# Kernel tuning notes

Hardware: AMD Instinct MI355X
Metric: run time of the kernel (lower is better)

The kernel has to match this reference:

```python
import jax, jax.numpy as jnp
import numpy as np

HIDDEN = 1024
NUM_HEADS = 16
HEAD_SIZE = HIDDEN // NUM_HEADS


def setup_inputs() -> dict:
    key = jax.random.key(0)
    ks = jax.random.split(key, 5)
    B, S = 2, 2048
    x = jax.random.normal(ks[0], (B, S, HIDDEN), dtype=jnp.float32)
    # nn.Linear(hidden, 3*hidden): weight stored (in, out) for x @ W
    scale_qkv = 1.0 / np.sqrt(HIDDEN)
    w_qkv = jax.random.uniform(ks[1], (HIDDEN, 3 * HIDDEN), minval=-scale_qkv, maxval=scale_qkv, dtype=jnp.float32)
    b_qkv = jax.random.uniform(ks[2], (3 * HIDDEN,), minval=-scale_qkv, maxval=scale_qkv, dtype=jnp.float32)
    w_o = jax.random.uniform(ks[3], (HIDDEN, HIDDEN), minval=-scale_qkv, maxval=scale_qkv, dtype=jnp.float32)
    b_o = jax.random.uniform(ks[4], (HIDDEN,), minval=-scale_qkv, maxval=scale_qkv, dtype=jnp.float32)
    return {"x": x, "w_qkv": w_qkv, "b_qkv": b_qkv, "w_o": w_o, "b_o": b_o}


def reference(x, w_qkv, b_qkv, w_o, b_o):
    B, S, H = x.shape
    qkv = x @ w_qkv + b_qkv  # (B, S, 3H)
    q, k, v = jnp.split(qkv, 3, axis=-1)
    # (B, S, H) -> (B, nheads, S, head_size)
    def heads(t):
        return t.reshape(B, S, NUM_HEADS, HEAD_SIZE).transpose(0, 2, 1, 3)
    q, k, v = heads(q), heads(k), heads(v)
    scores = jnp.einsum('bhqd,bhkd->bhqk', q, k) / np.sqrt(HEAD_SIZE).astype(np.float32)
    causal = jnp.tril(jnp.ones((S, S), dtype=bool))  # k <= q
    scores = jnp.where(causal, scores, -jnp.inf)
    probs = jax.nn.softmax(scores, axis=-1)
    out = jnp.einsum('bhqk,bhkd->bqhd', probs, v).reshape(B, S, H)
    return out @ w_o + b_o
```

## Files before the change

kernel.cpp:

```cpp
#include <hip/hip_runtime.h>
#include <stdint.h>


typedef __bf16 bf16;
typedef __attribute__((ext_vector_type(8))) __bf16 bf16x8;
typedef __attribute__((ext_vector_type(4))) __bf16 bf16x4;
typedef __attribute__((ext_vector_type(4))) float floatx4;
typedef __attribute__((ext_vector_type(16))) float floatx16;
typedef __attribute__((ext_vector_type(4))) unsigned int uint4v;
typedef __attribute__((ext_vector_type(2))) unsigned int uint2v;

#define SCL 0.18033688011112042f

__device__ __forceinline__ floatx4 mfma_bf16(bf16x8 a, bf16x8 b, floatx4 c) {
  return __builtin_amdgcn_mfma_f32_16x16x32_bf16(a, b, c, 0, 0, 0);
}

__device__ __forceinline__ floatx16 mfma32(bf16x8 a, bf16x8 b, floatx16 c) {
  return __builtin_amdgcn_mfma_f32_32x32x16_bf16(a, b, c, 0, 0, 0);
}

__device__ __forceinline__ void cp_g2l_16(const bf16* g, bf16* l) {
  __builtin_amdgcn_global_load_lds(
      (const __attribute__((address_space(1))) void*)g,
      (__attribute__((address_space(3))) void*)l, 16, 0, 0);
}

__device__ __forceinline__ floatx16 zero16() {
  floatx16 z;
#pragma unroll
  for (int i = 0; i < 16; ++i) z[i] = 0.f;
  return z;
}

__device__ __forceinline__ uint32_t pack2(float lo, float hi2) {
  union { bf16 h[2]; uint32_t u; } x;
  x.h[0] = (bf16)lo; x.h[1] = (bf16)hi2;
  return x.u;
}

__device__ __forceinline__ uint2v permswap(uint32_t a, uint32_t b) {
  return __builtin_amdgcn_permlane32_swap(a, b, false, false);
}

__device__ __forceinline__ bf16x8 mk_pf(uint32_t w0, uint32_t w1, uint32_t w2,
                                        uint32_t w3) {
  union { uint4v u; bf16x8 v; } c;
  c.u = (uint4v){w0, w1, w2, w3};
  return c.v;
}

__global__ __launch_bounds__(256) void prep_kernel(
    const float* __restrict__ x, bf16* __restrict__ xb,
    const float* __restrict__ w_qkv, bf16* __restrict__ wqkvt,
    const float* __restrict__ w_o, bf16* __restrict__ wot) {
  const int b = blockIdx.x;
  const int tid = threadIdx.x;
  if (b < 4096) {
    const int i = (b * 256 + tid) * 4;
    floatx4 v = *(const floatx4*)(x + i);
    bf16x4 o;
    o[0] = (bf16)v[0]; o[1] = (bf16)v[1]; o[2] = (bf16)v[2]; o[3] = (bf16)v[3];
    *(bf16x4*)(xb + i) = o;
    return;
  }
  __shared__ float tile[32][33];
  const float* W; bf16* Wt; int K, N, n0, k0;
  if (b < 7168) {
    const int bb = b - 4096;
    W = w_qkv; Wt = wqkvt; K = 1024; N = 3072;
    n0 = (bb % 96) * 32; k0 = (bb / 96) * 32;
  } else {
    const int bb = b - 7168;
    W = w_o; Wt = wot; K = 1024; N = 1024;
    n0 = (bb & 31) * 32; k0 = (bb >> 5) * 32;
  }
  const int tx = tid & 31, ty = tid >> 5;
  for (int i = 0; i < 4; ++i)
    tile[ty + 8 * i][tx] = W[(size_t)(k0 + ty + 8 * i) * N + n0 + tx];
  __syncthreads();
  for (int i = 0; i < 4; ++i)
    Wt[(size_t)(n0 + ty + 8 * i) * K + k0 + tx] = (bf16)tile[tx][ty + 8 * i];
}

template <int MODE, int MI>
__global__ __launch_bounds__(256, 3) void gemm_bt_kernel(
    const bf16* __restrict__ A, const bf16* __restrict__ Bt,
    const float* __restrict__ bias, float* __restrict__ outF,
    bf16* __restrict__ qb, bf16* __restrict__ kb, bf16* __restrict__ vtb,
    int N, int K) {
  constexpr int BM = MI * 32;
  __shared__ bf16 As[BM * 32];
  __shared__ bf16 Bs[128 * 32];
  const int tid = threadIdx.x;
  const int w = tid >> 6, lane = tid & 63;
  const int l16 = lane & 15, quad = lane >> 4;
  const int m0 = blockIdx.y * BM, n0 = blockIdx.x * 128;
  const int wm = (w & 1) * (BM / 2), wn = (w >> 1) * 64;

  const int r4 = lane >> 2, c4 = lane & 3;
  const int jj = (c4 - r4 - (r4 >> 2)) & 3;
  const int arow = w * (BM / 4) + r4;
  const bf16* Ag = A + (size_t)(m0 + arow) * K + jj * 8;
  bf16* Al = As + arow * 32 + c4 * 8;
  const int brow = w * 32 + r4;
  const bf16* Bg = Bt + (size_t)(n0 + brow) * K + jj * 8;
  bf16* Bl = Bs + brow * 32 + c4 * 8;

  floatx4 acc[MI][4];
#pragma unroll
  for (int i = 0; i < MI; ++i)
#pragma unroll
    for (int j = 0; j < 4; ++j) acc[i][j] = (floatx4){0.f, 0.f, 0.f, 0.f};

  for (int k0 = 0; k0 < K; k0 += 32) {
    __syncthreads();
    cp_g2l_16(Ag + k0, Al);
    if (MI == 4) cp_g2l_16(Ag + (size_t)16 * K + k0, Al + 16 * 32);
    cp_g2l_16(Bg + k0, Bl);
    cp_g2l_16(Bg + (size_t)16 * K + k0, Bl + 16 * 32);
    __syncthreads();
    bf16x8 af[MI], bfr[4];
#pragma unroll
    for (int i = 0; i < MI; ++i) {
      const int R = wm + i * 16 + l16;
      af[i] = *(const bf16x8*)(&As[R * 32 + ((quad + R + (R >> 2)) & 3) * 8]);
    }
#pragma unroll
    for (int j = 0; j < 4; ++j) {
      const int Rb = wn + j * 16 + l16;
      bfr[j] = *(const bf16x8*)(&Bs[Rb * 32 + ((quad + Rb + (Rb >> 2)) & 3) * 8]);
    }
#pragma unroll
    for (int i = 0; i < MI; ++i)
#pragma unroll
      for (int j = 0; j < 4; ++j)
        acc[i][j] = mfma_bf16(af[i], bfr[j], acc[i][j]);
  }

#pragma unroll
  for (int i = 0; i < MI; ++i)
#pragma unroll
    for (int j = 0; j < 4; ++j) {
      const int nn = n0 + wn + j * 16 + l16;
      const float bv = bias[nn];
      const int mbase = m0 + wm + i * 16 + quad * 4;
      if (MODE == 1) {
#pragma unroll
        for (int r = 0; r < 4; ++r)
          outF[(size_t)(mbase + r) * N + nn] = acc[i][j][r] + bv;
      } else {
        const int which = nn >> 10;
        const int rem = nn & 1023;
        const int h = rem >> 6, d = rem & 63;
        const int b = mbase >> 11, s = mbase & 2047;
        const size_t bh = (size_t)(b * 16 + h);
        if (which == 2) {
          bf16x4 pk;
#pragma unroll
          for (int r = 0; r < 4; ++r) pk[r] = (bf16)(acc[i][j][r] + bv);
          *(bf16x4*)(vtb + (bh * 64 + d) * 2048 + s) = pk;
        } else if (which == 0) {
#pragma unroll
          for (int r = 0; r < 4; ++r)
            qb[(bh * 2048 + s + r) * 64 + d] = (bf16)((acc[i][j][r] + bv) * SCL);
        } else {
#pragma unroll
          for (int r = 0; r < 4; ++r)
            kb[(bh * 2048 + s + r) * 64 + d] = (bf16)(acc[i][j][r] + bv);
        }
      }
    }
}

__global__ __launch_bounds__(256, 4) void attn_kernel(
    const bf16* __restrict__ Qb, const bf16* __restrict__ Kb,
    const bf16* __restrict__ Vtb, bf16* __restrict__ attnb) {
  __shared__ bf16 Ks[3][4096];
  __shared__ bf16 Vs[2][4096];
  const int bid = blockIdx.x;
  const int c = bid & 255, qq = bid >> 8;
  const int bh = c & 31;
  const int kk = c >> 5;
  const int g = (qq == 0) ? kk : (qq == 1) ? 31 - kk
              : (qq == 2) ? 8 + kk : 23 - kk;
  const int tid = threadIdx.x;
  const int w = tid >> 6, lane = tid & 63;
  const int l31 = lane & 31, hi = lane >> 5;
  const int strip = w >> 1, ms = w & 1;
  const int q0s = g * 64 + strip * 32;
  const int b = bh >> 4, h = bh & 15;
  const int nt = g + 1;

  const bf16* Qh = Qb + (size_t)bh * 2048 * 64;
  const bf16* Kh = Kb + (size_t)bh * 2048 * 64;
  const bf16* Vh = Vtb + (size_t)bh * 64 * 2048;

  const int c0 = tid, c1 = tid + 256;
  const int kof0 = (c0 >> 3) * 64 + ((((c0 & 7) - (c0 >> 3)) & 7) * 8);
  const int kof1 = (c1 >> 3) * 64 + ((((c1 & 7) - (c1 >> 3)) & 7) * 8);
  const int vof0 = (c0 >> 3) * 2048 + ((((c0 & 7) - (c0 >> 3)) & 7) * 8);
  const int vof1 = (c1 >> 3) * 2048 + ((((c1 & 7) - (c1 >> 3)) & 7) * 8);

  bf16x8 qf[4];
  {
    const bf16* Qr = Qh + (size_t)(q0s + l31) * 64 + hi * 8;
#pragma unroll
    for (int kd = 0; kd < 4; ++kd) qf[kd] = *(const bf16x8*)(Qr + kd * 16);
  }
  bf16x8 ones;
#pragma unroll
  for (int j = 0; j < 8; ++j) ones[j] = (bf16)1.0f;

  floatx16 O0 = zero16(), O1 = zero16(), Ol = zero16();

  {
    const int k1 = (1 < nt) ? 1 : 0;
    cp_g2l_16(Kh + kof0, &Ks[0][c0 * 8]);
    cp_g2l_16(Kh + kof1, &Ks[0][c1 * 8]);
    cp_g2l_16(Kh + (size_t)k1 * 4096 + kof0, &Ks[1][c0 * 8]);
    cp_g2l_16(Kh + (size_t)k1 * 4096 + kof1, &Ks[1][c1 * 8]);
    cp_g2l_16(Vh + vof0, &Vs[0][c0 * 8]);
    cp_g2l_16(Vh + vof1, &Vs[0][c1 * 8]);
    asm volatile("s_waitcnt vmcnt(4)" ::: "memory");
    __builtin_amdgcn_sched_barrier(0);
  }

  int kr = 0;
  for (int t = 0; t < nt; ++t) {
    __builtin_amdgcn_s_barrier();
    __builtin_amdgcn_sched_barrier(0);

    {
      const int tk = (t + 2 < nt) ? t + 2 : 0;
      const int tv = (t + 1 < nt) ? t + 1 : 0;
      const int kst = (kr >= 1) ? kr - 1 : 2;
      cp_g2l_16(Kh + (size_t)tk * 4096 + kof0, &Ks[kst][c0 * 8]);
      cp_g2l_16(Kh + (size_t)tk * 4096 + kof1, &Ks[kst][c1 * 8]);
      cp_g2l_16(Vh + (size_t)tv * 64 + vof0, &Vs[(t + 1) & 1][c0 * 8]);
      cp_g2l_16(Vh + (size_t)tv * 64 + vof1, &Vs[(t + 1) & 1][c1 * 8]);
    }

    const bool diag = (t == g);
    if (!(diag && strip == 0 && ms == 1)) {
      const bf16* KsC = &Ks[kr][0];

      floatx16 sf = zero16();
      const int row = ms * 32 + l31;
      __builtin_amdgcn_s_setprio(1);
#pragma unroll
      for (int kd = 0; kd < 4; ++kd) {
        bf16x8 kf = *(const bf16x8*)(
            &KsC[row * 64 + (((kd * 2 + hi) + row) & 7) * 8]);
        sf = mfma32(kf, qf[kd], sf);
      }
      __builtin_amdgcn_s_setprio(0);

      float e[16];
#pragma unroll
      for (int r = 0; r < 16; ++r) {
        float s = sf[r];
        if (diag) {
          const int kc = t * 64 + ms * 32 + (r & 3) + 8 * (r >> 2) + 4 * hi;
          s = (kc <= q0s + l31) ? s : -1e30f;
        }
        e[r] = __builtin_amdgcn_exp2f(s);
      }

      uint32_t W[8];
#pragma unroll
      for (int i = 0; i < 8; ++i) W[i] = pack2(e[2 * i], e[2 * i + 1]);
      uint2v s0 = permswap(W[0], W[2]);
      uint2v s1 = permswap(W[1], W[3]);
      bf16x8 pa = mk_pf(s0.x, s1.x, s0.y, s1.y);
      uint2v s2 = permswap(W[4], W[6]);
      uint2v s3 = permswap(W[5], W[7]);
      bf16x8 pb = mk_pf(s2.x, s3.x, s2.y, s3.y);

      asm volatile("s_waitcnt vmcnt(4)" ::: "memory");
      __builtin_amdgcn_sched_barrier(0);

      const bf16* VsC = &Vs[t & 1][0];
      const int ksA = ms * 2, ksB = ms * 2 + 1;
      const int r0 = l31, r1 = 32 + l31;
      bf16x8 va0 = *(const bf16x8*)(&VsC[r0 * 64 + (((ksA * 2 + hi) + r0) & 7) * 8]);
      bf16x8 va1 = *(const bf16x8*)(&VsC[r1 * 64 + (((ksA * 2 + hi) + r1) & 7) * 8]);
      bf16x8 vb0 = *(const bf16x8*)(&VsC[r0 * 64 + (((ksB * 2 + hi) + r0) & 7) * 8]);
      bf16x8 vb1 = *(const bf16x8*)(&VsC[r1 * 64 + (((ksB * 2 + hi) + r1) & 7) * 8]);

      __builtin_amdgcn_s_setprio(1);
      O0 = mfma32(pa, va0, O0);
      O1 = mfma32(pa, va1, O1);
      Ol = mfma32(pa, ones, Ol);
      O0 = mfma32(pb, vb0, O0);
      O1 = mfma32(pb, vb1, O1);
      Ol = mfma32(pb, ones, Ol);
      __builtin_amdgcn_s_setprio(0);
    }
    kr = (kr == 2) ? 0 : kr + 1;
  }

  __syncthreads();
  float* fO = (float*)(&Ks[0][0]);
  float* fL = (float*)(&Vs[0][0]);
  if (ms == 1) {
#pragma unroll
    for (int r = 0; r < 16; ++r) {
      const int ql = (r & 3) + 8 * (r >> 2) + 4 * hi;
      fO[strip * 2048 + ql * 64 + l31] = O0[r];
      fO[strip * 2048 + ql * 64 + 32 + l31] = O1[r];
      if (l31 == 0) fL[strip * 32 + ql] = Ol[r];
    }
  }
  __syncthreads();
  if (ms == 0) {
#pragma unroll
    for (int r = 0; r < 16; ++r) {
      const int ql = (r & 3) + 8 * (r >> 2) + 4 * hi;
      const float o0 = O0[r] + fO[strip * 2048 + ql * 64 + l31];
      const float o1 = O1[r] + fO[strip * 2048 + ql * 64 + 32 + l31];
      const float inv = 1.f / (Ol[r] + fL[strip * 32 + ql]);
      bf16* dst = attnb + ((size_t)(b * 2048 + q0s + ql)) * 1024 + h * 64;
      dst[l31] = (bf16)(o0 * inv);
      dst[32 + l31] = (bf16)(o1 * inv);
    }
  }
}

extern "C" void kernel_launch(void* const* d_in, const int* in_sizes, int n_in,
                              void* d_out, int out_size, void* d_ws, size_t ws_size,
                              hipStream_t stream) {
  const float* x     = (const float*)d_in[0];
  const float* w_qkv = (const float*)d_in[1];
  const float* b_qkv = (const float*)d_in[2];
  const float* w_o   = (const float*)d_in[3];
  const float* b_o   = (const float*)d_in[4];
  float* out = (float*)d_out;

  char* ws = (char*)d_ws;
  bf16* xb    = (bf16*)ws; ws += (size_t)4096 * 1024 * 2;
  bf16* wqkvt = (bf16*)ws; ws += (size_t)3072 * 1024 * 2;
  bf16* wot   = (bf16*)ws; ws += (size_t)1024 * 1024 * 2;
  bf16* qb    = (bf16*)ws; ws += (size_t)32 * 2048 * 64 * 2;
  bf16* kb    = (bf16*)ws; ws += (size_t)32 * 2048 * 64 * 2;
  bf16* vtb   = (bf16*)ws; ws += (size_t)32 * 2048 * 64 * 2;
  bf16* attnb = (bf16*)ws; ws += (size_t)4096 * 1024 * 2;

  prep_kernel<<<8192, 256, 0, stream>>>(x, xb, w_qkv, wqkvt, w_o, wot);
  gemm_bt_kernel<0, 4><<<dim3(24, 32), 256, 0, stream>>>(
      xb, wqkvt, b_qkv, nullptr, qb, kb, vtb, 3072, 1024);
  attn_kernel<<<1024, 256, 0, stream>>>(qb, kb, vtb, attnb);
  gemm_bt_kernel<1, 2><<<dim3(8, 64), 256, 0, stream>>>(
      attnb, wot, b_o, out, nullptr, nullptr, nullptr, 1024, 1024);
}
```

Measured before the change: 171.2 us.

## Software-pipeline PV MFMAs by one tile to overlap with QK and exp

The P·V MFMAs for tile t-1 are deferred into iteration t, so they sit between the QK^T MFMAs and the exp/pack work of tile t, with a drain after the loop. The V fragments for the previous tile are read from LDS right after the barrier. The goal is to hide the exp/pack latency and LDS read latency behind independent matrix work instead of serialising QK, softmax and PV within each iteration. In exchange, P must stay live across iterations, which costs registers. V is read from the buffer that the next prefetch overwrites in the same iteration, and only the barrier before those reads orders them against other waves' async loads, so there is a possible LDS read/write race.

```diff
diff --git a/kernel.cpp b/kernel.cpp
--- a/kernel.cpp
+++ b/kernel.cpp
@@ -226,9 +226,23 @@
     __builtin_amdgcn_sched_barrier(0);
   }
 
+  const int ksA = ms * 2, ksB = ms * 2 + 1;
+  const int r0v = l31, r1v = 32 + l31;
+  bf16x8 paS, pbS;
+  int havePrev = 0;
   int kr = 0;
   for (int t = 0; t < nt; ++t) {
     __builtin_amdgcn_s_barrier();
+    __builtin_amdgcn_sched_barrier(0);
+
+    bf16x8 va0, va1, vb0, vb1;
+    if (havePrev) {
+      const bf16* VsP = &Vs[(t - 1) & 1][0];
+      va0 = *(const bf16x8*)(&VsP[r0v * 64 + (((ksA * 2 + hi) + r0v) & 7) * 8]);
+      va1 = *(const bf16x8*)(&VsP[r1v * 64 + (((ksA * 2 + hi) + r1v) & 7) * 8]);
+      vb0 = *(const bf16x8*)(&VsP[r0v * 64 + (((ksB * 2 + hi) + r0v) & 7) * 8]);
+      vb1 = *(const bf16x8*)(&VsP[r1v * 64 + (((ksB * 2 + hi) + r1v) & 7) * 8]);
+    }
     __builtin_amdgcn_sched_barrier(0);
 
     {
@@ -242,10 +256,12 @@
     }
 
     const bool diag = (t == g);
-    if (!(diag && strip == 0 && ms == 1)) {
+    const bool skip = diag && strip == 0 && ms == 1;
+
+    floatx16 sf;
+    if (!skip) {
+      sf = zero16();
       const bf16* KsC = &Ks[kr][0];
-
-      floatx16 sf = zero16();
       const int row = ms * 32 + l31;
       __builtin_amdgcn_s_setprio(1);
 #pragma unroll
@@ -255,7 +271,20 @@
         sf = mfma32(kf, qf[kd], sf);
       }
       __builtin_amdgcn_s_setprio(0);
-
+    }
+
+    if (havePrev) {
+      __builtin_amdgcn_s_setprio(1);
+      O0 = mfma32(paS, va0, O0);
+      O1 = mfma32(paS, va1, O1);
+      Ol = mfma32(paS, ones, Ol);
+      O0 = mfma32(pbS, vb0, O0);
+      O1 = mfma32(pbS, vb1, O1);
+      Ol = mfma32(pbS, ones, Ol);
+      __builtin_amdgcn_s_setprio(0);
+    }
+
+    if (!skip) {
       float e[16];
 #pragma unroll
       for (int r = 0; r < 16; ++r) {
@@ -266,38 +295,37 @@
         }
         e[r] = __builtin_amdgcn_exp2f(s);
       }
-
       uint32_t W[8];
 #pragma unroll
       for (int i = 0; i < 8; ++i) W[i] = pack2(e[2 * i], e[2 * i + 1]);
       uint2v s0 = permswap(W[0], W[2]);
       uint2v s1 = permswap(W[1], W[3]);
-      bf16x8 pa = mk_pf(s0.x, s1.x, s0.y, s1.y);
+      paS = mk_pf(s0.x, s1.x, s0.y, s1.y);
       uint2v s2 = permswap(W[4], W[6]);
       uint2v s3 = permswap(W[5], W[7]);
-      bf16x8 pb = mk_pf(s2.x, s3.x, s2.y, s3.y);
-
-      asm volatile("s_waitcnt vmcnt(4)" ::: "memory");
-      __builtin_amdgcn_sched_barrier(0);
-
-      const bf16* VsC = &Vs[t & 1][0];
-      const int ksA = ms * 2, ksB = ms * 2 + 1;
-      const int r0 = l31, r1 = 32 + l31;
-      bf16x8 va0 = *(const bf16x8*)(&VsC[r0 * 64 + (((ksA * 2 + hi) + r0) & 7) * 8]);
-      bf16x8 va1 = *(const bf16x8*)(&VsC[r1 * 64 + (((ksA * 2 + hi) + r1) & 7) * 8]);
-      bf16x8 vb0 = *(const bf16x8*)(&VsC[r0 * 64 + (((ksB * 2 + hi) + r0) & 7) * 8]);
-      bf16x8 vb1 = *(const bf16x8*)(&VsC[r1 * 64 + (((ksB * 2 + hi) + r1) & 7) * 8]);
-
-      __builtin_amdgcn_s_setprio(1);
-      O0 = mfma32(pa, va0, O0);
-      O1 = mfma32(pa, va1, O1);
-      Ol = mfma32(pa, ones, Ol);
-      O0 = mfma32(pb, vb0, O0);
-      O1 = mfma32(pb, vb1, O1);
-      Ol = mfma32(pb, ones, Ol);
-      __builtin_amdgcn_s_setprio(0);
-    }
+      pbS = mk_pf(s2.x, s3.x, s2.y, s3.y);
+      havePrev = 1;
+    } else {
+      havePrev = 0;
+    }
+
+    asm volatile("s_waitcnt vmcnt(4)" ::: "memory");
+    __builtin_amdgcn_sched_barrier(0);
     kr = (kr == 2) ? 0 : kr + 1;
+  }
+
+  if (havePrev) {
+    const bf16* VsP = &Vs[(nt - 1) & 1][0];
+    bf16x8 va0 = *(const bf16x8*)(&VsP[r0v * 64 + (((ksA * 2 + hi) + r0v) & 7) * 8]);
+    bf16x8 va1 = *(const bf16x8*)(&VsP[r1v * 64 + (((ksA * 2 + hi) + r1v) & 7) * 8]);
+    bf16x8 vb0 = *(const bf16x8*)(&VsP[r0v * 64 + (((ksB * 2 + hi) + r0v) & 7) * 8]);
+    bf16x8 vb1 = *(const bf16x8*)(&VsP[r1v * 64 + (((ksB * 2 + hi) + r1v) & 7) * 8]);
+    O0 = mfma32(paS, va0, O0);
+    O1 = mfma32(paS, va1, O1);
+    Ol = mfma32(paS, ones, Ol);
+    O0 = mfma32(pbS, vb0, O0);
+    O1 = mfma32(pbS, vb1, O1);
+    Ol = mfma32(pbS, ones, Ol);
   }
 
   __syncthreads();
```

After: 197.6 us. 15.5% more time.
